# Kernel optimization log

Measured on AMD Instinct MI355X. Metric: run time of the kernel, lower is better.

The kernel has to match this reference:

```python
import jax, jax.numpy as jnp
import numpy as np

R_CUT = 10.0
ROUNDS = 1  # num_message_passing_rounds


def setup_inputs() -> dict:
    key = jax.random.key(0)
    N, DEG, S, NRBF, G = 10000, 16, 128, 20, 64
    E = N * DEG
    ks = jax.random.split(key, 16)
    w = lambda k, shp, fan: (jax.random.normal(k, shp, dtype=jnp.float32) / np.float32(np.sqrt(fan)))
    return {
        "edge_vector_diffs": jax.random.normal(ks[0], (E, 3), dtype=jnp.float32) * 3.0,
        "edge_lengths": jax.random.uniform(ks[1], (E,), dtype=jnp.float32) * 15.0,
        "node_from": jnp.repeat(jnp.arange(N), DEG),            # every node has DEG outgoing edges
        "node_graph_index": jax.random.randint(ks[2], (N,), 0, G),
        "num_graphs": G,
        "emb0": jax.random.normal(ks[3], (S,), dtype=jnp.float32) * 0.01,  # embedding.weight[0]
        "phi_w1": w(ks[4], (S, S), S), "phi_b1": jnp.zeros((S,), jnp.float32),
        "phi_w2": w(ks[5], (S, 3 * S), S), "phi_b2": jnp.zeros((3 * S,), jnp.float32),
        "filt_w": w(ks[6], (NRBF, 3 * S), NRBF), "filt_b": jnp.zeros((3 * S,), jnp.float32),
        "u_w": w(ks[7], (S, S), S), "v_w": w(ks[8], (S, S), S),
        "upd_w1": w(ks[9], (2 * S, S), 2 * S), "upd_b1": jnp.zeros((S,), jnp.float32),
        "upd_w2": w(ks[10], (S, 3 * S), S), "upd_b2": jnp.zeros((3 * S,), jnp.float32),
        "out_w1": w(ks[11], (S, S), S), "out_b1": jnp.zeros((S,), jnp.float32),
        "out_w2": w(ks[12], (S, 1), S), "out_b2": jnp.zeros((1,), jnp.float32),
    }


def reference(edge_vector_diffs, edge_lengths, node_from, node_graph_index, num_graphs,
              emb0, phi_w1, phi_b1, phi_w2, phi_b2, filt_w, filt_b, u_w, v_w,
              upd_w1, upd_b1, upd_w2, upd_b2, out_w1, out_b1, out_w2, out_b2):
    S = phi_w1.shape[0]
    N = node_graph_index.shape[0]
    NRBF = filt_w.shape[0]
    silu = jax.nn.silu
    seg = lambda v, n: jax.ops.segment_sum(v, node_from, num_segments=n)

    mask = (jnp.abs(edge_lengths) <= R_CUT).astype(jnp.float32)          # [E] nbr_mask
    r = jnp.linalg.norm(edge_vector_diffs, axis=1)                        # [E]
    r_safe = jnp.maximum(r, 1e-12)
    k = jnp.arange(1, NRBF + 1, dtype=jnp.float32)
    # PAINN sinc radial basis sin(k*pi*r/r_cut)/r, then linear -> [E, 3S]
    rbf = jnp.sin(k[None, :] * jnp.pi * r_safe[:, None] / R_CUT) / r_safe[:, None]
    cutoff = 0.5 * (jnp.cos(jnp.pi * r / R_CUT) + 1.0) * (r < R_CUT)      # cosine cutoff
    W = (rbf @ filt_w + filt_b) * cutoff[:, None]                          # [E, 3S]

    tile3 = jnp.arange(S) % 3  # xyzxyz... truncation pattern from .repeat(...)[: S]
    # scalar Frobenius norm of each node's masked neighbor-diff block
    frob = jnp.sqrt(seg(mask * r * r, N))                                  # [N]
    denom_e = frob[node_from]
    denom_e = jnp.where(denom_e > 0, denom_e, 1.0)
    normalized = edge_vector_diffs / denom_e[:, None]                      # [E, 3]
    norm_exp = normalized[:, tile3]                                        # [E, S]

    # state init: sum over dim 1 of embedding(zeros) == S * embedding.weight[0]
    state = jnp.broadcast_to(jnp.float32(S) * emb0, (N, S))
    state_vec = jnp.zeros((N, 3, S), jnp.float32)

    for _ in range(ROUNDS):
        # message block (nbrs_node_from == destination node, so sync update == original sequential loop)
        phi = silu(state[node_from] @ phi_w1 + phi_b1) @ phi_w2 + phi_b2   # [E, 3S]
        prod = phi * W
        m1, m2, m3 = prod[:, :S], prod[:, S:2 * S], prod[:, 2 * S:]
        vec_msg = state_vec[node_from] * m1[:, None, :] + (norm_exp * m3)[:, None, :]  # [E,3,S]
        state = seg(m2 * mask[:, None], N)                                 # [N, S]
        state_vec = seg(vec_msg * mask[:, None, None], N)                  # [N, 3, S]
        # update block
        U = jnp.einsum('nps,st->npt', state_vec, u_w)                      # [N,3,S]
        V = jnp.einsum('nps,st->npt', state_vec, v_w)
        UV = jnp.einsum('nps,nqs->npq', U, V)                              # [N,3,3]
        Vnorm = jnp.sqrt(jnp.sum(V * V, axis=1))                           # [N,S]
        a = silu(jnp.concatenate([Vnorm, state], axis=-1) @ upd_w1 + upd_b1) @ upd_w2 + upd_b2
        a_vv, a_sv, a_ss = a[:, :S], a[:, S:2 * S], a[:, 2 * S:]
        uv_tiled = jnp.sum(UV, axis=1)[:, tile3]                           # [N,S]
        state = a_ss + uv_tiled * a_sv
        state_vec = U * a_vv[:, None, :]

    graph_state = jax.ops.segment_sum(state, node_graph_index, num_segments=num_graphs)
    out = (silu(graph_state @ out_w1 + out_b1) @ out_w2 + out_b2).ravel()  # [num_graphs]
    return out
```

## Files before the change

### kernel.cpp

```cpp
#include <hip/hip_runtime.h>
#include <math.h>

#define NN   10000
#define DEG  16
#define SS   128
#define NRBF 20
#define GG   64
#define RC   10.0f
#define PI_F 3.14159265358979323846f
#define NB   4

__device__ __forceinline__ float silu_f(float x){
    return x / (1.0f + __expf(-x));
}

__global__ __launch_bounds__(256) void k_phi1(
    const float* __restrict__ emb0,
    const float* __restrict__ w1, const float* __restrict__ b1,
    float* __restrict__ phiH, float* __restrict__ gs){
    __shared__ float s0[SS];
    __shared__ float part[2][SS];
    int t = threadIdx.x;
    for (int i = t; i < GG*SS; i += 256) gs[i] = 0.0f;
    if (t < SS) s0[t] = 128.0f * emb0[t];
    __syncthreads();
    int c = t & 127, half = t >> 7;
    float acc = 0.0f;
    int s0i = half * 64;
    #pragma unroll 8
    for (int s = 0; s < 64; s++)
        acc = fmaf(s0[s0i + s], w1[(s0i + s)*SS + c], acc);
    part[half][c] = acc;
    __syncthreads();
    if (t < SS) phiH[t] = silu_f(b1[t] + part[0][t] + part[1][t]);
}

__global__ __launch_bounds__(128) void k_phi2(
    const float* __restrict__ phiH,
    const float* __restrict__ w2, const float* __restrict__ b2,
    float* __restrict__ phiW){
    __shared__ float hL[SS];
    __shared__ float part[4][32];
    int t = threadIdx.x;
    hL[t] = phiH[t];
    __syncthreads();
    int c  = blockIdx.x*32 + (t & 31);
    int kk = t >> 5;
    float acc = 0.0f;
    int sbase = kk * 32;
    #pragma unroll 8
    for (int s = 0; s < 32; s++)
        acc = fmaf(hL[sbase + s], w2[(sbase + s)*3*SS + c], acc);
    part[kk][t & 31] = acc;
    __syncthreads();
    if (t < 32){
        int cc = blockIdx.x*32 + t;
        phiW[cc] = b2[cc] + part[0][t] + part[1][t] + part[2][t] + part[3][t];
    }
}

__global__ __launch_bounds__(128) void k_edge(
    const float* __restrict__ evd, const float* __restrict__ elen,
    const int* __restrict__ node_from,
    const float* __restrict__ filt_w, const float* __restrict__ filt_b,
    const float* __restrict__ phiW,
    float* __restrict__ state, float* __restrict__ sv){
    __shared__ float rS[DEG];
    __shared__ float mcL[DEG];
    __shared__ float frL[DEG];
    __shared__ float eV[DEG][3];
    __shared__ float rbfL[DEG][NRBF];
    __shared__ float invD;
    int n = blockIdx.x;
    int t = threadIdx.x;

    if (t < DEG){
        int e = n*DEG + t;
        float x = evd[3*e+0], y = evd[3*e+1], z = evd[3*e+2];
        float r = sqrtf(x*x + y*y + z*z);
        float len  = elen[e];
        float mask = (fabsf(len) <= RC) ? 1.0f : 0.0f;
        float cut  = (r < RC) ? 0.5f*(cosf(PI_F*r*(1.0f/RC)) + 1.0f) : 0.0f;
        rS[t]  = fmaxf(r, 1e-12f);
        mcL[t] = mask * cut;
        frL[t] = mask * r * r;
        eV[t][0] = x; eV[t][1] = y; eV[t][2] = z;
    }
    __syncthreads();
    for (int idx = t; idx < DEG*NRBF; idx += 128){
        int e = idx / NRBF, k = idx % NRBF;
        float rs = rS[e];
        rbfL[e][k] = sinf((float)(k+1) * (PI_F/RC) * rs) / rs;
    }
    if (t == 0){
        float s = 0.0f;
        for (int e = 0; e < DEG; e++) s += frL[e];
        float fbn = sqrtf(s);
        invD = (fbn > 0.0f) ? 1.0f/fbn : 1.0f;
    }
    __syncthreads();

    int gc1 = SS + t;
    int gc2 = 2*SS + t;
    float fw1[NRBF], fw2[NRBF];
    #pragma unroll
    for (int k = 0; k < NRBF; k++){
        fw1[k] = filt_w[k*(3*SS) + gc1];
        fw2[k] = filt_w[k*(3*SS) + gc2];
    }
    float fb1 = filt_b[gc1], fb2 = filt_b[gc2];
    float ph1 = phiW[gc1],   ph2 = phiW[gc2];
    float iD  = invD;
    int   s3  = t % 3;

    float acc1 = 0.0f, acc2 = 0.0f;
    for (int e = 0; e < DEG; e++){
        float mc = mcL[e];
        if (mc == 0.0f) continue;
        const float4* rv = (const float4*)(&rbfL[e][0]);
        float4 r0 = rv[0], r1 = rv[1], r2 = rv[2], r3 = rv[3], r4 = rv[4];
        float rr[20] = {r0.x,r0.y,r0.z,r0.w, r1.x,r1.y,r1.z,r1.w,
                        r2.x,r2.y,r2.z,r2.w, r3.x,r3.y,r3.z,r3.w,
                        r4.x,r4.y,r4.z,r4.w};
        float w1 = fb1, w2 = fb2;
        #pragma unroll
        for (int k = 0; k < NRBF; k++){
            w1 = fmaf(rr[k], fw1[k], w1);
            w2 = fmaf(rr[k], fw2[k], w2);
        }
        acc1 = fmaf(ph1*mc, w1, acc1);
        acc2 = fmaf(ph2*mc*eV[e][s3]*iD, w2, acc2);
    }
    int nf = node_from[n*DEG];
    state[nf*SS + t] = acc1;
    sv[nf*SS + t]    = acc2;
}

__global__ __launch_bounds__(128) void k_update(
    const float* __restrict__ state, const float* __restrict__ sv,
    const float* __restrict__ u_w, const float* __restrict__ v_w,
    const float* __restrict__ upd_w1, const float* __restrict__ upd_b1,
    const float* __restrict__ upd_w2, const float* __restrict__ upd_b2,
    const int* __restrict__ ngi, float* __restrict__ gs){
    __shared__ __align__(16) float svT[SS][NB];
    __shared__ __align__(16) float xT[2*SS][NB];
    __shared__ __align__(16) float h2T[SS][NB];
    __shared__ float red[2][NB];
    __shared__ float dL[NB];
    int t  = threadIdx.x;
    int n0 = blockIdx.x * NB;

    for (int idx = t; idx < NB*SS; idx += 128){
        int b = idx >> 7, s = idx & (SS-1);
        svT[s][b]     = sv[(n0+b)*SS + s];
        xT[SS+s][b]   = state[(n0+b)*SS + s];
    }
    __syncthreads();

    float accU[NB], accV[NB];
    #pragma unroll
    for (int b = 0; b < NB; b++){ accU[b]=0.f; accV[b]=0.f; }
    for (int s = 0; s < SS; s++){
        float wu = u_w[s*SS + t];
        float wv = v_w[s*SS + t];
        float4 s03 = *((const float4*)(&svT[s][0]));
        float svv[NB] = {s03.x,s03.y,s03.z,s03.w};
        #pragma unroll
        for (int b = 0; b < NB; b++){
            accU[b] = fmaf(svv[b], wu, accU[b]);
            accV[b] = fmaf(svv[b], wv, accV[b]);
        }
    }

    int lane = t & 63, wid = t >> 6;
    #pragma unroll
    for (int b = 0; b < NB; b++){
        float p = accU[b]*accV[b];
        for (int off = 32; off; off >>= 1) p += __shfl_down(p, off);
        if (lane == 0) red[wid][b] = p;
    }
    {
        float4 q0;
        q0.x = sqrtf(3.f*accV[0]*accV[0]); q0.y = sqrtf(3.f*accV[1]*accV[1]);
        q0.z = sqrtf(3.f*accV[2]*accV[2]); q0.w = sqrtf(3.f*accV[3]*accV[3]);
        ((float4*)(&xT[t][0]))[0] = q0;
    }
    __syncthreads();
    if (t < NB) dL[t] = red[0][t] + red[1][t];

    float accH[NB];
    #pragma unroll
    for (int b = 0; b < NB; b++) accH[b] = 0.f;
    for (int i = 0; i < 2*SS; i++){
        float w = upd_w1[i*SS + t];
        float4 x03 = *((const float4*)(&xT[i][0]));
        float xv[NB] = {x03.x,x03.y,x03.z,x03.w};
        #pragma unroll
        for (int b = 0; b < NB; b++) accH[b] = fmaf(xv[b], w, accH[b]);
    }
    float b1v = upd_b1[t];
    {
        float4 q0;
        q0.x = silu_f(accH[0]+b1v); q0.y = silu_f(accH[1]+b1v);
        q0.z = silu_f(accH[2]+b1v); q0.w = silu_f(accH[3]+b1v);
        ((float4*)(&h2T[t][0]))[0] = q0;
    }
    __syncthreads();

    float a1[NB], a2[NB];
    #pragma unroll
    for (int b = 0; b < NB; b++){ a1[b]=0.f; a2[b]=0.f; }
    for (int j = 0; j < SS; j++){
        float w1 = upd_w2[j*3*SS + SS   + t];
        float w2 = upd_w2[j*3*SS + 2*SS + t];
        float4 h03 = *((const float4*)(&h2T[j][0]));
        float hv[NB] = {h03.x,h03.y,h03.z,h03.w};
        #pragma unroll
        for (int b = 0; b < NB; b++){
            a1[b] = fmaf(hv[b], w1, a1[b]);
            a2[b] = fmaf(hv[b], w2, a2[b]);
        }
    }
    float bsv = upd_b2[SS+t], bss = upd_b2[2*SS+t];
    #pragma unroll
    for (int b = 0; b < NB; b++){
        float ns = (a2[b] + bss) + 3.0f*dL[b]*(a1[b] + bsv);
        int g = ngi[n0+b];
        atomicAdd(&gs[g*SS + t], ns);
    }
}

__global__ __launch_bounds__(128) void k_out(
    const float* __restrict__ gs,
    const float* __restrict__ w1, const float* __restrict__ b1,
    const float* __restrict__ w2, const float* __restrict__ b2,
    float* __restrict__ out){
    __shared__ float gsL[SS];
    __shared__ float red[2];
    int g = blockIdx.x, t = threadIdx.x;
    gsL[t] = gs[g*SS + t];
    __syncthreads();
    float acc = b1[t];
    #pragma unroll 4
    for (int s = 0; s < SS; s++) acc = fmaf(gsL[s], w1[s*SS + t], acc);
    float p = silu_f(acc) * w2[t];
    for (int off = 32; off; off >>= 1) p += __shfl_down(p, off);
    if ((t & 63) == 0) red[t >> 6] = p;
    __syncthreads();
    if (t == 0) out[g] = red[0] + red[1] + b2[0];
}

extern "C" void kernel_launch(void* const* d_in, const int* in_sizes, int n_in,
                              void* d_out, int out_size, void* d_ws, size_t ws_size,
                              hipStream_t stream) {
    const float* evd     = (const float*)d_in[0];
    const float* elen    = (const float*)d_in[1];
    const int*   nfrom   = (const int*)  d_in[2];
    const int*   ngi     = (const int*)  d_in[3];
    const float* emb0    = (const float*)d_in[5];
    const float* phi_w1  = (const float*)d_in[6];
    const float* phi_b1  = (const float*)d_in[7];
    const float* phi_w2  = (const float*)d_in[8];
    const float* phi_b2  = (const float*)d_in[9];
    const float* filt_w  = (const float*)d_in[10];
    const float* filt_b  = (const float*)d_in[11];
    const float* u_w     = (const float*)d_in[12];
    const float* v_w     = (const float*)d_in[13];
    const float* upd_w1  = (const float*)d_in[14];
    const float* upd_b1  = (const float*)d_in[15];
    const float* upd_w2  = (const float*)d_in[16];
    const float* upd_b2  = (const float*)d_in[17];
    const float* out_w1  = (const float*)d_in[18];
    const float* out_b1  = (const float*)d_in[19];
    const float* out_w2  = (const float*)d_in[20];
    const float* out_b2  = (const float*)d_in[21];

    float* ws    = (float*)d_ws;
    float* phiW  = ws;
    float* state = ws + 512;
    float* sv    = state + NN*SS;
    float* gs    = sv + NN*SS;
    float* phiH  = gs + GG*SS;

    k_phi1<<<1, 256, 0, stream>>>(emb0, phi_w1, phi_b1, phiH, gs);
    k_phi2<<<12, 128, 0, stream>>>(phiH, phi_w2, phi_b2, phiW);
    k_edge<<<NN, 128, 0, stream>>>(evd, elen, nfrom, filt_w, filt_b, phiW, state, sv);
    k_update<<<NN/NB, 128, 0, stream>>>(state, sv, u_w, v_w,
                                        upd_w1, upd_b1, upd_w2, upd_b2, ngi, gs);
    k_out<<<GG, 128, 0, stream>>>(gs, out_w1, out_b1, out_w2, out_b2, (float*)d_out);
}
```

Baseline: 180.8 us.

## Register-tile update kernel over 2 nodes by 4 columns with 8 nodes per block

The update kernel now handles 8 nodes per block instead of 4. Each thread computes a 2-node by 4-column register tile, using float4 weight loads and float2 shared-memory reads, across the U/V projection and both update MLP layers. The dot-product reduction now uses 32-lane sub-wave shuffles, one per node pair. The aim is to halve the global weight traffic per node and raise arithmetic intensity, at the cost of half as many blocks and more registers per thread.

```diff
diff --git a/kernel.cpp b/kernel.cpp
--- a/kernel.cpp
+++ b/kernel.cpp
@@ -8,7 +8,7 @@
 #define GG   64
 #define RC   10.0f
 #define PI_F 3.14159265358979323846f
-#define NB   4
+#define NB   8
 
 __device__ __forceinline__ float silu_f(float x){
     return x / (1.0f + __expf(-x));
@@ -145,88 +145,127 @@
     __shared__ __align__(16) float svT[SS][NB];
     __shared__ __align__(16) float xT[2*SS][NB];
     __shared__ __align__(16) float h2T[SS][NB];
-    __shared__ float red[2][NB];
     __shared__ float dL[NB];
     int t  = threadIdx.x;
+    int cq = t & 31;
+    int c0 = cq * 4;
+    int pr = t >> 5;
     int n0 = blockIdx.x * NB;
 
     for (int idx = t; idx < NB*SS; idx += 128){
         int b = idx >> 7, s = idx & (SS-1);
-        svT[s][b]     = sv[(n0+b)*SS + s];
-        xT[SS+s][b]   = state[(n0+b)*SS + s];
-    }
-    __syncthreads();
-
-    float accU[NB], accV[NB];
-    #pragma unroll
-    for (int b = 0; b < NB; b++){ accU[b]=0.f; accV[b]=0.f; }
+        svT[s][b]   = sv[(n0+b)*SS + s];
+        xT[SS+s][b] = state[(n0+b)*SS + s];
+    }
+    __syncthreads();
+
+    float accU[2][4], accV[2][4];
+    #pragma unroll
+    for (int b = 0; b < 2; b++)
+        #pragma unroll
+        for (int j = 0; j < 4; j++){ accU[b][j]=0.f; accV[b][j]=0.f; }
+    #pragma unroll 2
     for (int s = 0; s < SS; s++){
-        float wu = u_w[s*SS + t];
-        float wv = v_w[s*SS + t];
-        float4 s03 = *((const float4*)(&svT[s][0]));
-        float svv[NB] = {s03.x,s03.y,s03.z,s03.w};
-        #pragma unroll
-        for (int b = 0; b < NB; b++){
-            accU[b] = fmaf(svv[b], wu, accU[b]);
-            accV[b] = fmaf(svv[b], wv, accV[b]);
+        float4 wu = *((const float4*)(u_w + s*SS + c0));
+        float4 wv = *((const float4*)(v_w + s*SS + c0));
+        float wua[4] = {wu.x,wu.y,wu.z,wu.w};
+        float wva[4] = {wv.x,wv.y,wv.z,wv.w};
+        float2 s2 = *((const float2*)(&svT[s][pr*2]));
+        float sn[2] = {s2.x, s2.y};
+        #pragma unroll
+        for (int b = 0; b < 2; b++)
+            #pragma unroll
+            for (int j = 0; j < 4; j++){
+                accU[b][j] = fmaf(sn[b], wua[j], accU[b][j]);
+                accV[b][j] = fmaf(sn[b], wva[j], accV[b][j]);
+            }
+    }
+
+    float du[2];
+    #pragma unroll
+    for (int b = 0; b < 2; b++){
+        du[b] = accU[b][0]*accV[b][0] + accU[b][1]*accV[b][1]
+              + accU[b][2]*accV[b][2] + accU[b][3]*accV[b][3];
+    }
+    #pragma unroll
+    for (int off = 16; off; off >>= 1){
+        du[0] += __shfl_down(du[0], off, 32);
+        du[1] += __shfl_down(du[1], off, 32);
+    }
+    if (cq == 0){ dL[pr*2] = du[0]; dL[pr*2+1] = du[1]; }
+
+    #pragma unroll
+    for (int j = 0; j < 4; j++){
+        xT[c0+j][pr*2+0] = sqrtf(3.f*accV[0][j]*accV[0][j]);
+        xT[c0+j][pr*2+1] = sqrtf(3.f*accV[1][j]*accV[1][j]);
+    }
+    __syncthreads();
+
+    float accH[2][4];
+    #pragma unroll
+    for (int b = 0; b < 2; b++)
+        #pragma unroll
+        for (int j = 0; j < 4; j++) accH[b][j] = 0.f;
+    #pragma unroll 2
+    for (int i = 0; i < 2*SS; i++){
+        float4 w = *((const float4*)(upd_w1 + i*SS + c0));
+        float wa[4] = {w.x,w.y,w.z,w.w};
+        float2 x2 = *((const float2*)(&xT[i][pr*2]));
+        float xv[2] = {x2.x, x2.y};
+        #pragma unroll
+        for (int b = 0; b < 2; b++)
+            #pragma unroll
+            for (int j = 0; j < 4; j++)
+                accH[b][j] = fmaf(xv[b], wa[j], accH[b][j]);
+    }
+    {
+        float4 b1q = *((const float4*)(upd_b1 + c0));
+        float b1a[4] = {b1q.x,b1q.y,b1q.z,b1q.w};
+        #pragma unroll
+        for (int j = 0; j < 4; j++){
+            h2T[c0+j][pr*2+0] = silu_f(accH[0][j] + b1a[j]);
+            h2T[c0+j][pr*2+1] = silu_f(accH[1][j] + b1a[j]);
         }
     }
-
-    int lane = t & 63, wid = t >> 6;
-    #pragma unroll
-    for (int b = 0; b < NB; b++){
-        float p = accU[b]*accV[b];
-        for (int off = 32; off; off >>= 1) p += __shfl_down(p, off);
-        if (lane == 0) red[wid][b] = p;
+    __syncthreads();
+
+    float a1[2][4], a2[2][4];
+    #pragma unroll
+    for (int b = 0; b < 2; b++)
+        #pragma unroll
+        for (int j = 0; j < 4; j++){ a1[b][j]=0.f; a2[b][j]=0.f; }
+    #pragma unroll 2
+    for (int s = 0; s < SS; s++){
+        float4 wa4 = *((const float4*)(upd_w2 + s*3*SS + SS   + c0));
+        float4 wb4 = *((const float4*)(upd_w2 + s*3*SS + 2*SS + c0));
+        float waa[4] = {wa4.x,wa4.y,wa4.z,wa4.w};
+        float wba[4] = {wb4.x,wb4.y,wb4.z,wb4.w};
+        float2 h2 = *((const float2*)(&h2T[s][pr*2]));
+        float hv[2] = {h2.x, h2.y};
+        #pragma unroll
+        for (int b = 0; b < 2; b++)
+            #pragma unroll
+            for (int j = 0; j < 4; j++){
+                a1[b][j] = fmaf(hv[b], waa[j], a1[b][j]);
+                a2[b][j] = fmaf(hv[b], wba[j], a2[b][j]);
+            }
     }
     {
-        float4 q0;
-        q0.x = sqrtf(3.f*accV[0]*accV[0]); q0.y = sqrtf(3.f*accV[1]*accV[1]);
-        q0.z = sqrtf(3.f*accV[2]*accV[2]); q0.w = sqrtf(3.f*accV[3]*accV[3]);
-        ((float4*)(&xT[t][0]))[0] = q0;
-    }
-    __syncthreads();
-    if (t < NB) dL[t] = red[0][t] + red[1][t];
-
-    float accH[NB];
-    #pragma unroll
-    for (int b = 0; b < NB; b++) accH[b] = 0.f;
-    for (int i = 0; i < 2*SS; i++){
-        float w = upd_w1[i*SS + t];
-        float4 x03 = *((const float4*)(&xT[i][0]));
-        float xv[NB] = {x03.x,x03.y,x03.z,x03.w};
-        #pragma unroll
-        for (int b = 0; b < NB; b++) accH[b] = fmaf(xv[b], w, accH[b]);
-    }
-    float b1v = upd_b1[t];
-    {
-        float4 q0;
-        q0.x = silu_f(accH[0]+b1v); q0.y = silu_f(accH[1]+b1v);
-        q0.z = silu_f(accH[2]+b1v); q0.w = silu_f(accH[3]+b1v);
-        ((float4*)(&h2T[t][0]))[0] = q0;
-    }
-    __syncthreads();
-
-    float a1[NB], a2[NB];
-    #pragma unroll
-    for (int b = 0; b < NB; b++){ a1[b]=0.f; a2[b]=0.f; }
-    for (int j = 0; j < SS; j++){
-        float w1 = upd_w2[j*3*SS + SS   + t];
-        float w2 = upd_w2[j*3*SS + 2*SS + t];
-        float4 h03 = *((const float4*)(&h2T[j][0]));
-        float hv[NB] = {h03.x,h03.y,h03.z,h03.w};
-        #pragma unroll
-        for (int b = 0; b < NB; b++){
-            a1[b] = fmaf(hv[b], w1, a1[b]);
-            a2[b] = fmaf(hv[b], w2, a2[b]);
+        float4 bsvq = *((const float4*)(upd_b2 + SS   + c0));
+        float4 bssq = *((const float4*)(upd_b2 + 2*SS + c0));
+        float bsva[4] = {bsvq.x,bsvq.y,bsvq.z,bsvq.w};
+        float bssa[4] = {bssq.x,bssq.y,bssq.z,bssq.w};
+        #pragma unroll
+        for (int b = 0; b < 2; b++){
+            int node = pr*2 + b;
+            float d3 = 3.0f * dL[node];
+            int g = ngi[n0 + node];
+            #pragma unroll
+            for (int j = 0; j < 4; j++){
+                float ns = (a2[b][j] + bssa[j]) + d3*(a1[b][j] + bsva[j]);
+                atomicAdd(&gs[g*SS + c0 + j], ns);
+            }
         }
-    }
-    float bsv = upd_b2[SS+t], bss = upd_b2[2*SS+t];
-    #pragma unroll
-    for (int b = 0; b < NB; b++){
-        float ns = (a2[b] + bss) + 3.0f*dL[b]*(a1[b] + bsv);
-        int g = ngi[n0+b];
-        atomicAdd(&gs[g*SS + t], ns);
     }
 }
 
```

New measurement: 230.4 us. 27.4% more time.
